# Optimization experiments

Measured on AMD Instinct MI355X. Metric: run time of the kernel, lower is better.

The kernel has to match this reference:

```python
import jax, jax.numpy as jnp
import numpy as np

B = 8192      # sessions
L = 64        # tokens per session
T = B * L     # total tokens
H = 128       # hidden_size
MAX_LEN = 64  # position_emb has MAX_LEN+1 rows


def setup_inputs() -> dict:
    key = jax.random.key(0)
    ks = jax.random.split(key, 10)
    s1 = 1.0 / np.sqrt(H)
    s2 = 1.0 / np.sqrt(2 * H)
    hidden = jax.random.normal(ks[0], (T, H), jnp.float32)
    seq_len = jnp.full((B,), L, dtype=jnp.int32)
    # reversed positions 1..L within each session (<= MAX_LEN)
    reverse_pos = jnp.tile(jnp.arange(L, 0, -1, dtype=jnp.int32), B)
    return {
        "hidden": hidden,
        "pos_table": jax.random.normal(ks[1], (MAX_LEN + 1, H), jnp.float32) * 0.02,
        "W_pos_w": jax.random.normal(ks[2], (H, 2 * H), jnp.float32) * s2,
        "W_pos_b": jax.random.normal(ks[3], (H,), jnp.float32) * s2,
        "W1_w": jax.random.normal(ks[4], (H, H), jnp.float32) * s1,
        "W1_b": jax.random.normal(ks[5], (H,), jnp.float32) * s1,
        "W2_w": jax.random.normal(ks[6], (H, H), jnp.float32) * s1,
        "W2_b": jax.random.normal(ks[7], (H,), jnp.float32) * s1,
        "q_w": jax.random.normal(ks[8], (1, H), jnp.float32) * s1,
        "q_b": jax.random.normal(ks[9], (1,), jnp.float32) * s1,
        "seq_len": seq_len,
        "reverse_pos": reverse_pos,
    }


def reference(hidden, pos_table, W_pos_w, W_pos_b, W1_w, W1_b, W2_w, W2_b,
              q_w, q_b, seq_len, reverse_pos):
    Bn = seq_len.shape[0]
    Tn = hidden.shape[0]
    # token -> session id (replaces the python split loop)
    seg = jnp.repeat(jnp.arange(Bn), seq_len, total_repeat_length=Tn)  # [T]
    # per-session mean, broadcast back to tokens (v_mean_repeat_concat)
    mean = jax.ops.segment_sum(hidden, seg, num_segments=Bn) \
        / seq_len[:, None].astype(hidden.dtype)                        # [B,H]
    mean_rep = mean[seg]                                               # [T,H]
    pos_emb = pos_table[reverse_pos]                                   # [T,H]
    pos_hidden = jnp.tanh(
        jnp.concatenate([hidden, pos_emb], axis=-1) @ W_pos_w.T + W_pos_b
    )                                                                  # [T,H]
    gate = jax.nn.sigmoid(mean_rep @ W1_w.T + W1_b + pos_hidden @ W2_w.T + W2_b)
    alpha = gate @ q_w.T + q_b                                         # [T,1]
    # per-session sum of alpha-weighted tokens (h_s)
    return jax.ops.segment_sum(alpha * hidden, seg, num_segments=Bn)   # [B,H]
```

## Files before the change

### kernel.cpp

```cpp
#include <hip/hip_runtime.h>
#include <hip/hip_bf16.h>

typedef unsigned short u16;
typedef __bf16 bf16x8 __attribute__((ext_vector_type(8)));
typedef float  f32x4  __attribute__((ext_vector_type(4)));

__device__ __forceinline__ unsigned pk2(float a, float b) {
    __hip_bfloat162 h = __float22bfloat162_rn(make_float2(a, b));
    unsigned u; __builtin_memcpy(&u, &h, 4);
    return u;
}
__device__ __forceinline__ u16 f2b1(float f) { return (u16)(pk2(f, f) & 0xFFFFu); }

#define MFMA __builtin_amdgcn_mfma_f32_16x16x32_bf16

__global__ __launch_bounds__(128) void prep_kernel(
    const float* __restrict__ pos_table, const float* __restrict__ Wpw,
    const float* __restrict__ Wpb, const float* __restrict__ W2,
    float* __restrict__ ppK, u16* __restrict__ wb1, u16* __restrict__ wb2)
{
    const int b = blockIdx.x, t = threadIdx.x;
    if (b < 65) {
        const float4* pr = (const float4*)(pos_table + b * 128);
        const float4* wr = (const float4*)(Wpw + t * 256 + 128);
        float acc = Wpb[t];
        #pragma unroll
        for (int k = 0; k < 32; ++k) {
            const float4 p = pr[k], wv = wr[k];
            acc += p.x * wv.x + p.y * wv.y + p.z * wv.z + p.w * wv.w;
        }
        ppK[b * 128 + t] = acc * 2.885390081777927f;
    } else {
        const int j = b - 65;
        wb1[j * 128 + t] = f2b1(Wpw[j * 256 + t]);
        wb2[j * 128 + t] = f2b1(W2[j * 128 + t]);
    }
}

__global__ __launch_bounds__(256, 2) void fused_kernel(
    const float* __restrict__ hidden, const int* __restrict__ rpos,
    const float* __restrict__ W1, const float* __restrict__ W1b,
    const float* __restrict__ W2b, const float* __restrict__ qw,
    const float* __restrict__ qb, const float* __restrict__ ppK,
    const u16* __restrict__ wb1g, const u16* __restrict__ wb2g,
    float* __restrict__ out)
{
    __shared__ __align__(16) u16 hbf[128 * 136];
    __shared__ __align__(16) u16 wb[128 * 136];
    __shared__ float meanv[256];
    __shared__ float g1s[256];
    __shared__ float qws[128];
    __shared__ float alphas[128];
    __shared__ int   rps[128];

    const int tid = threadIdx.x;
    const int blk = blockIdx.x;
    const int w = tid >> 6;
    const int l = tid & 63;
    const int c = l & 15;
    const int g = l >> 4;
    const int R = 32 * w;
    const float* hsrc = hidden + (size_t)blk * (128 * 128);

    meanv[tid] = 0.f;
    if (tid < 128) { rps[tid] = rpos[blk * 128 + tid]; qws[tid] = qw[tid]; }
    __syncthreads();

    {
        float4 ms0 = {0.f, 0.f, 0.f, 0.f}, ms1 = {0.f, 0.f, 0.f, 0.f};
        #pragma unroll
        for (int i = 0; i < 16; ++i) {
            const int i4 = tid + i * 256;
            const float4 v = ((const float4*)hsrc)[i4];
            const int e = i4 * 4, row = e >> 7, col = e & 127;
            uint2 st; st.x = pk2(v.x, v.y); st.y = pk2(v.z, v.w);
            *(uint2*)&hbf[row * 136 + col] = st;
            if (i < 8) { ms0.x += v.x; ms0.y += v.y; ms0.z += v.z; ms0.w += v.w; }
            else       { ms1.x += v.x; ms1.y += v.y; ms1.z += v.z; ms1.w += v.w; }
        }
        const int mc = (tid * 4) & 127;
        atomicAdd(&meanv[mc],           ms0.x); atomicAdd(&meanv[mc + 1],       ms0.y);
        atomicAdd(&meanv[mc + 2],       ms0.z); atomicAdd(&meanv[mc + 3],       ms0.w);
        atomicAdd(&meanv[128 + mc],     ms1.x); atomicAdd(&meanv[128 + mc + 1], ms1.y);
        atomicAdd(&meanv[128 + mc + 2], ms1.z); atomicAdd(&meanv[128 + mc + 3], ms1.w);
    }
    #pragma unroll
    for (int i = 0; i < 8; ++i) {
        const int ch = tid + i * 256;
        const int e = ch * 8, row = e >> 7, col = e & 127;
        *(uint4*)&wb[row * 136 + col] = ((const uint4*)wb1g)[ch];
    }
    __syncthreads();

    {
        const int col = tid & 127, s = tid >> 7;
        const float4* wr = (const float4*)(W1 + col * 128);
        const float4* mv = (const float4*)(meanv + s * 128);
        float acc = 0.f;
        #pragma unroll 8
        for (int k4 = 0; k4 < 32; ++k4) {
            const float4 wv = wr[k4], m4 = mv[k4];
            acc += m4.x * wv.x + m4.y * wv.y + m4.z * wv.z + m4.w * wv.w;
        }
        g1s[tid] = W1b[col] + W2b[col] + acc * (1.f / 64.f);
    }

    bf16x8 af[2][4];
    #pragma unroll
    for (int m = 0; m < 2; ++m)
        #pragma unroll
        for (int kk = 0; kk < 4; ++kk)
            af[m][kk] = *(const bf16x8*)&hbf[(R + 16 * m + c) * 136 + kk * 32 + g * 8];
    f32x4 acc1[2][8] = {};
    #pragma unroll
    for (int n = 0; n < 8; ++n) {
        #pragma unroll
        for (int kk = 0; kk < 4; ++kk) {
            const bf16x8 bfr = *(const bf16x8*)&wb[(16 * n + c) * 136 + kk * 32 + g * 8];
            acc1[0][n] = MFMA(af[0][kk], bfr, acc1[0][n], 0, 0, 0);
            acc1[1][n] = MFMA(af[1][kk], bfr, acc1[1][n], 0, 0, 0);
        }
    }
    {
        const float K2 = 2.885390081777927f;
        const float* pkp[2][4];
        #pragma unroll
        for (int m = 0; m < 2; ++m)
            #pragma unroll
            for (int r = 0; r < 4; ++r)
                pkp[m][r] = ppK + rps[R + 16 * m + 4 * g + r] * 128 + c;
        #pragma unroll
        for (int m = 0; m < 2; ++m)
            #pragma unroll
            for (int n = 0; n < 8; ++n)
                #pragma unroll
                for (int r = 0; r < 4; ++r) {
                    const float arg = fmaf(acc1[m][n][r], K2, pkp[m][r][16 * n]);
                    const float e2 = __builtin_amdgcn_exp2f(arg);
                    const float rc = __builtin_amdgcn_rcpf(e2 + 1.f);
                    const float th = fmaf(-2.f, rc, 1.f);
                    hbf[(R + 16 * m + 4 * g + r) * 136 + 16 * n + c] = f2b1(th);
                }
    }
    __syncthreads();

    bf16x8 af2[2][4];
    #pragma unroll
    for (int m = 0; m < 2; ++m)
        #pragma unroll
        for (int kk = 0; kk < 4; ++kk)
            af2[m][kk] = *(const bf16x8*)&hbf[(R + 16 * m + c) * 136 + kk * 32 + g * 8];
    #pragma unroll
    for (int i = 0; i < 8; ++i) {
        const int ch = tid + i * 256;
        const int e = ch * 8, row = e >> 7, col = e & 127;
        *(uint4*)&wb[row * 136 + col] = ((const uint4*)wb2g)[ch];
    }
    __syncthreads();

    f32x4 acc2[2][8] = {};
    #pragma unroll
    for (int n = 0; n < 8; ++n) {
        #pragma unroll
        for (int kk = 0; kk < 4; ++kk) {
            const bf16x8 bfr = *(const bf16x8*)&wb[(16 * n + c) * 136 + kk * 32 + g * 8];
            acc2[0][n] = MFMA(af2[0][kk], bfr, acc2[0][n], 0, 0, 0);
            acc2[1][n] = MFMA(af2[1][kk], bfr, acc2[1][n], 0, 0, 0);
        }
    }
    {
        const float K1 = 1.4426950408889634f;
        const int sw = w >> 1;
        float garr[8], qarr[8];
        #pragma unroll
        for (int n = 0; n < 8; ++n) {
            garr[n] = -K1 * g1s[sw * 128 + 16 * n + c];
            qarr[n] = qws[16 * n + c];
        }
        float prt[2][4] = {};
        #pragma unroll
        for (int m = 0; m < 2; ++m)
            #pragma unroll
            for (int n = 0; n < 8; ++n)
                #pragma unroll
                for (int r = 0; r < 4; ++r) {
                    const float arg = fmaf(acc2[m][n][r], -K1, garr[n]);
                    const float e2 = __builtin_amdgcn_exp2f(arg);
                    const float rc = __builtin_amdgcn_rcpf(e2 + 1.f);
                    prt[m][r] = fmaf(rc, qarr[n], prt[m][r]);
                }
        #pragma unroll
        for (int msk = 1; msk <= 8; msk <<= 1)
            #pragma unroll
            for (int m = 0; m < 2; ++m)
                #pragma unroll
                for (int r = 0; r < 4; ++r)
                    prt[m][r] += __shfl_xor(prt[m][r], msk, 64);
        if (c == 0) {
            const float qbv = qb[0];
            #pragma unroll
            for (int m = 0; m < 2; ++m)
                #pragma unroll
                for (int r = 0; r < 4; ++r)
                    alphas[R + 16 * m + 4 * g + r] = prt[m][r] + qbv;
        }
    }
    __syncthreads();

    {
        const int h = tid & 127, p = tid >> 7;
        const float* hs = hsrc + p * (64 * 128) + h;
        float accf = 0.f;
        #pragma unroll 8
        for (int t = 0; t < 64; ++t)
            accf = fmaf(alphas[64 * p + t], hs[t * 128], accf);
        out[(size_t)blk * 256 + tid] = accf;
    }
}

extern "C" void kernel_launch(void* const* d_in, const int* in_sizes, int n_in,
                              void* d_out, int out_size, void* d_ws, size_t ws_size,
                              hipStream_t stream)
{
    const float* hidden    = (const float*)d_in[0];
    const float* pos_table = (const float*)d_in[1];
    const float* Wpw       = (const float*)d_in[2];
    const float* Wpb       = (const float*)d_in[3];
    const float* W1w       = (const float*)d_in[4];
    const float* W1b       = (const float*)d_in[5];
    const float* W2w       = (const float*)d_in[6];
    const float* W2b       = (const float*)d_in[7];
    const float* qw        = (const float*)d_in[8];
    const float* qb        = (const float*)d_in[9];
    const int*   rpos      = (const int*)d_in[11];
    float* out = (float*)d_out;

    const int B = in_sizes[10];

    char* wsb = (char*)d_ws;
    float* ppK = (float*)wsb;
    u16* wb1   = (u16*)(wsb + 33280);
    u16* wb2   = (u16*)(wsb + 33280 + 32768);

    prep_kernel<<<193, 128, 0, stream>>>(pos_table, Wpw, Wpb, W2w,
                                         ppK, wb1, wb2);
    fused_kernel<<<B / 2, 256, 0, stream>>>(hidden, rpos, W1w, W1b, W2b, qw, qb,
                                            ppK, wb1, wb2, out);
}
```

Measured before the change: 486.5 us.

## Read MFMA weight fragments from global in pre-swizzled layout, drop weight LDS tile

The prep kernel now stores the bf16 W_pos and W2 matrices in a fragment-ordered layout, so each lane can load its MFMA B operand straight from global/L2 instead of staging the weights through a 34KB shared-memory tile. Removing that tile halves LDS use, and launch bounds go from 2 to 4 blocks per CU to raise occupancy. The GEMM loops are restructured to finish one n-tile of accumulators at a time, cutting register pressure. The per-session mean atomics are also halved with a wave shuffle, and two barriers are removed. In exchange, every wave repeatedly reads weights from L2 rather than LDS, which adds latency on the critical MFMA path.

Result: no change. 481.4 us (-1.0%).

```diff
diff --git a/kernel.cpp b/kernel.cpp
--- a/kernel.cpp
+++ b/kernel.cpp
@@ -32,12 +32,13 @@
         ppK[b * 128 + t] = acc * 2.885390081777927f;
     } else {
         const int j = b - 65;
-        wb1[j * 128 + t] = f2b1(Wpw[j * 256 + t]);
-        wb2[j * 128 + t] = f2b1(W2[j * 128 + t]);
-    }
-}
-
-__global__ __launch_bounds__(256, 2) void fused_kernel(
+        const int off = (((j >> 4) * 4 + (t >> 5)) * 16 + (j & 15)) * 32 + (t & 31);
+        wb1[off] = f2b1(Wpw[j * 256 + t]);
+        wb2[off] = f2b1(W2[j * 128 + t]);
+    }
+}
+
+__global__ __launch_bounds__(256, 4) void fused_kernel(
     const float* __restrict__ hidden, const int* __restrict__ rpos,
     const float* __restrict__ W1, const float* __restrict__ W1b,
     const float* __restrict__ W2b, const float* __restrict__ qw,
@@ -46,7 +47,6 @@
     float* __restrict__ out)
 {
     __shared__ __align__(16) u16 hbf[128 * 136];
-    __shared__ __align__(16) u16 wb[128 * 136];
     __shared__ float meanv[256];
     __shared__ float g1s[256];
     __shared__ float qws[128];
@@ -78,17 +78,17 @@
             if (i < 8) { ms0.x += v.x; ms0.y += v.y; ms0.z += v.z; ms0.w += v.w; }
             else       { ms1.x += v.x; ms1.y += v.y; ms1.z += v.z; ms1.w += v.w; }
         }
-        const int mc = (tid * 4) & 127;
-        atomicAdd(&meanv[mc],           ms0.x); atomicAdd(&meanv[mc + 1],       ms0.y);
-        atomicAdd(&meanv[mc + 2],       ms0.z); atomicAdd(&meanv[mc + 3],       ms0.w);
-        atomicAdd(&meanv[128 + mc],     ms1.x); atomicAdd(&meanv[128 + mc + 1], ms1.y);
-        atomicAdd(&meanv[128 + mc + 2], ms1.z); atomicAdd(&meanv[128 + mc + 3], ms1.w);
-    }
-    #pragma unroll
-    for (int i = 0; i < 8; ++i) {
-        const int ch = tid + i * 256;
-        const int e = ch * 8, row = e >> 7, col = e & 127;
-        *(uint4*)&wb[row * 136 + col] = ((const uint4*)wb1g)[ch];
+        ms0.x += __shfl_xor(ms0.x, 32, 64); ms0.y += __shfl_xor(ms0.y, 32, 64);
+        ms0.z += __shfl_xor(ms0.z, 32, 64); ms0.w += __shfl_xor(ms0.w, 32, 64);
+        ms1.x += __shfl_xor(ms1.x, 32, 64); ms1.y += __shfl_xor(ms1.y, 32, 64);
+        ms1.z += __shfl_xor(ms1.z, 32, 64); ms1.w += __shfl_xor(ms1.w, 32, 64);
+        if ((l & 32) == 0) {
+            const int mc = (tid * 4) & 127;
+            atomicAdd(&meanv[mc],           ms0.x); atomicAdd(&meanv[mc + 1],       ms0.y);
+            atomicAdd(&meanv[mc + 2],       ms0.z); atomicAdd(&meanv[mc + 3],       ms0.w);
+            atomicAdd(&meanv[128 + mc],     ms1.x); atomicAdd(&meanv[128 + mc + 1], ms1.y);
+            atomicAdd(&meanv[128 + mc + 2], ms1.z); atomicAdd(&meanv[128 + mc + 3], ms1.w);
+        }
     }
     __syncthreads();
 
@@ -111,38 +111,38 @@
         #pragma unroll
         for (int kk = 0; kk < 4; ++kk)
             af[m][kk] = *(const bf16x8*)&hbf[(R + 16 * m + c) * 136 + kk * 32 + g * 8];
-    f32x4 acc1[2][8] = {};
+
+    int pko[2][4];
     #pragma unroll
-    for (int n = 0; n < 8; ++n) {
-        #pragma unroll
-        for (int kk = 0; kk < 4; ++kk) {
-            const bf16x8 bfr = *(const bf16x8*)&wb[(16 * n + c) * 136 + kk * 32 + g * 8];
-            acc1[0][n] = MFMA(af[0][kk], bfr, acc1[0][n], 0, 0, 0);
-            acc1[1][n] = MFMA(af[1][kk], bfr, acc1[1][n], 0, 0, 0);
-        }
-    }
-    {
+    for (int m = 0; m < 2; ++m)
+        #pragma unroll
+        for (int r = 0; r < 4; ++r)
+            pko[m][r] = rps[R + 16 * m + 4 * g + r] * 128 + c;
+
+    {
+        const u16* wb1p = wb1g + c * 32 + g * 8;
         const float K2 = 2.885390081777927f;
-        const float* pkp[2][4];
-        #pragma unroll
-        for (int m = 0; m < 2; ++m)
-            #pragma unroll
-            for (int r = 0; r < 4; ++r)
-                pkp[m][r] = ppK + rps[R + 16 * m + 4 * g + r] * 128 + c;
-        #pragma unroll
-        for (int m = 0; m < 2; ++m)
-            #pragma unroll
-            for (int n = 0; n < 8; ++n)
+        #pragma unroll
+        for (int n = 0; n < 8; ++n) {
+            f32x4 acc[2] = {};
+            #pragma unroll
+            for (int kk = 0; kk < 4; ++kk) {
+                const bf16x8 bfr = *(const bf16x8*)(wb1p + n * 2048 + kk * 512);
+                acc[0] = MFMA(af[0][kk], bfr, acc[0], 0, 0, 0);
+                acc[1] = MFMA(af[1][kk], bfr, acc[1], 0, 0, 0);
+            }
+            #pragma unroll
+            for (int m = 0; m < 2; ++m)
                 #pragma unroll
                 for (int r = 0; r < 4; ++r) {
-                    const float arg = fmaf(acc1[m][n][r], K2, pkp[m][r][16 * n]);
+                    const float arg = fmaf(acc[m][r], K2, ppK[pko[m][r] + 16 * n]);
                     const float e2 = __builtin_amdgcn_exp2f(arg);
                     const float rc = __builtin_amdgcn_rcpf(e2 + 1.f);
-                    const float th = fmaf(-2.f, rc, 1.f);
-                    hbf[(R + 16 * m + 4 * g + r) * 136 + 16 * n + c] = f2b1(th);
+                    hbf[(R + 16 * m + 4 * g + r) * 136 + 16 * n + c] =
+                        f2b1(fmaf(-2.f, rc, 1.f));
                 }
-    }
-    __syncthreads();
+        }
+    }
 
     bf16x8 af2[2][4];
     #pragma unroll
@@ -150,45 +150,35 @@
         #pragma unroll
         for (int kk = 0; kk < 4; ++kk)
             af2[m][kk] = *(const bf16x8*)&hbf[(R + 16 * m + c) * 136 + kk * 32 + g * 8];
-    #pragma unroll
-    for (int i = 0; i < 8; ++i) {
-        const int ch = tid + i * 256;
-        const int e = ch * 8, row = e >> 7, col = e & 127;
-        *(uint4*)&wb[row * 136 + col] = ((const uint4*)wb2g)[ch];
-    }
-    __syncthreads();
-
-    f32x4 acc2[2][8] = {};
-    #pragma unroll
-    for (int n = 0; n < 8; ++n) {
-        #pragma unroll
-        for (int kk = 0; kk < 4; ++kk) {
-            const bf16x8 bfr = *(const bf16x8*)&wb[(16 * n + c) * 136 + kk * 32 + g * 8];
-            acc2[0][n] = MFMA(af2[0][kk], bfr, acc2[0][n], 0, 0, 0);
-            acc2[1][n] = MFMA(af2[1][kk], bfr, acc2[1][n], 0, 0, 0);
-        }
-    }
-    {
+
+    __syncthreads();
+
+    {
+        const u16* wb2p = wb2g + c * 32 + g * 8;
         const float K1 = 1.4426950408889634f;
         const int sw = w >> 1;
-        float garr[8], qarr[8];
+        float prt[2][4] = {};
         #pragma unroll
         for (int n = 0; n < 8; ++n) {
-            garr[n] = -K1 * g1s[sw * 128 + 16 * n + c];
-            qarr[n] = qws[16 * n + c];
-        }
-        float prt[2][4] = {};
-        #pragma unroll
-        for (int m = 0; m < 2; ++m)
-            #pragma unroll
-            for (int n = 0; n < 8; ++n)
+            f32x4 acc[2] = {};
+            #pragma unroll
+            for (int kk = 0; kk < 4; ++kk) {
+                const bf16x8 bfr = *(const bf16x8*)(wb2p + n * 2048 + kk * 512);
+                acc[0] = MFMA(af2[0][kk], bfr, acc[0], 0, 0, 0);
+                acc[1] = MFMA(af2[1][kk], bfr, acc[1], 0, 0, 0);
+            }
+            const float gv = -K1 * g1s[sw * 128 + 16 * n + c];
+            const float qv = qws[16 * n + c];
+            #pragma unroll
+            for (int m = 0; m < 2; ++m)
                 #pragma unroll
                 for (int r = 0; r < 4; ++r) {
-                    const float arg = fmaf(acc2[m][n][r], -K1, garr[n]);
+                    const float arg = fmaf(acc[m][r], -K1, gv);
                     const float e2 = __builtin_amdgcn_exp2f(arg);
                     const float rc = __builtin_amdgcn_rcpf(e2 + 1.f);
-                    prt[m][r] = fmaf(rc, qarr[n], prt[m][r]);
+                    prt[m][r] = fmaf(rc, qv, prt[m][r]);
                 }
+        }
         #pragma unroll
         for (int msk = 1; msk <= 8; msk <<= 1)
             #pragma unroll
```
